# Kernel optimization log

Measured on AMD Instinct MI355X. Metric: run time of the kernel, lower is better.

## Reference

```python
import jax, jax.numpy as jnp
import numpy as np

B, N, C = 128, 2048, 3
VL, PN = 256, 128  # vector_length, prediction_num
NEG_SLOPE = 0.01   # torch LeakyReLU default
BN_EPS = 1e-5


def _lin(key, fin, fout):
    k1, k2 = jax.random.split(key)
    lim = 1.0 / np.sqrt(fin)
    W = jax.random.uniform(k1, (fin, fout), minval=-lim, maxval=lim, dtype=jnp.float32)
    b = jax.random.uniform(k2, (fout,), minval=-lim, maxval=lim, dtype=jnp.float32)
    return W, b


def setup_inputs() -> dict:
    key = jax.random.key(0)
    ks = jax.random.split(key, 14)
    x = jax.random.normal(ks[0], (B, N, C), dtype=jnp.float32)
    lengths = jnp.maximum(jax.random.randint(ks[1], (B,), 0, N), 1).astype(jnp.int32)
    eps = jax.random.normal(ks[2], (B, VL), dtype=jnp.float32)
    W1, b1 = _lin(ks[3], C, 64)
    W2, b2 = _lin(ks[4], 64, 64)
    W3, b3 = _lin(ks[5], 64, 128)
    W4, b4 = _lin(ks[6], 128, 1024)
    Wf, bf = _lin(ks[7], 1024, 1024)
    Wmu, bmu = _lin(ks[8], 1024, VL)
    Wlv, blv = _lin(ks[9], 1024, VL)
    Wd1, bd1 = _lin(ks[10], VL, 1024)
    Wd2, bd2 = _lin(ks[11], 1024, 1024)
    Wd3, bd3 = _lin(ks[12], 1024, PN * C)
    g1 = jnp.ones((1024,), jnp.float32); be1 = jnp.zeros((1024,), jnp.float32)
    g2 = jnp.ones((1024,), jnp.float32); be2 = jnp.zeros((1024,), jnp.float32)
    return dict(x=x, lengths=lengths, eps=eps,
                W1=W1, b1=b1, W2=W2, b2=b2, W3=W3, b3=b3, W4=W4, b4=b4,
                Wf=Wf, bf=bf, Wmu=Wmu, bmu=bmu, Wlv=Wlv, blv=blv,
                Wd1=Wd1, bd1=bd1, g1=g1, be1=be1,
                Wd2=Wd2, bd2=bd2, g2=g2, be2=be2,
                Wd3=Wd3, bd3=bd3)


def _lrelu(h):
    return jnp.where(h > 0, h, NEG_SLOPE * h)


def _bn(h, g, b):
    # BatchNorm1d in training mode: biased batch stats
    m = h.mean(axis=0)
    v = h.var(axis=0)
    return (h - m) * jax.lax.rsqrt(v + BN_EPS) * g + b


def reference(x, lengths, eps,
              W1, b1, W2, b2, W3, b3, W4, b4,
              Wf, bf, Wmu, bmu, Wlv, blv,
              Wd1, bd1, g1, be1, Wd2, bd2, g2, be2, Wd3, bd3):
    # --- pointnet per-point MLP (batched over padded [B,N,C]) ---
    h = _lrelu(x @ W1 + b1)          # [B,N,64]
    h = _lrelu(h @ W2 + b2)          # [B,N,64]
    h = _lrelu(h @ W3 + b3)          # [B,N,128]
    h = _lrelu(h @ W4 + b4)          # [B,N,1024]
    # masked max over points (ragged -> padded+mask)
    mask = jnp.arange(N)[None, :] < lengths[:, None]   # [B,N]
    h = jnp.where(mask[:, :, None], h, -jnp.inf)
    pooled = jnp.max(h, axis=1)      # [B,1024]
    # --- encoder head ---
    e = _lrelu(pooled @ Wf + bf)
    mu = e @ Wmu + bmu               # [B,VL]
    logvar = e @ Wlv + blv           # [B,VL]
    # --- reparameterize ---
    z = mu + eps * jnp.exp(0.5 * logvar)
    # --- decoder: Linear+BN+LeakyReLU x2, final Linear ---
    d = _lrelu(_bn(z @ Wd1 + bd1, g1, be1))
    d = _lrelu(_bn(d @ Wd2 + bd2, g2, be2))
    y = (d @ Wd3 + bd3).reshape(-1, PN, C)   # [B,PN,C]
    return (y, mu, logvar)
```

## Files before the change

### kernel.cpp

```cpp
#include <hip/hip_runtime.h>
#include <hip/hip_bf16.h>
#include <math.h>

#define NEG_SLOPE 0.01f

typedef short short8 __attribute__((ext_vector_type(8)));
typedef float f32x4 __attribute__((ext_vector_type(4)));

__device__ __forceinline__ float lrelu(float v) { return v > 0.0f ? v : NEG_SLOPE * v; }

__device__ __forceinline__ short f2bf(float f) {
    __hip_bfloat16 h = __float2bfloat16(f);
    return __builtin_bit_cast(short, h);
}

__global__ __launch_bounds__(256) void pack_all(
    const float* __restrict__ W4, const float* __restrict__ Wf,
    const float* __restrict__ Wmu, const float* __restrict__ Wlv,
    const float* __restrict__ Wd1, const float* __restrict__ Wd2,
    const float* __restrict__ Wd3, const float* __restrict__ W2,
    const float* __restrict__ W3,
    short* __restrict__ F4, short* __restrict__ Ff, short* __restrict__ Fmuvl,
    short* __restrict__ Fd1, short* __restrict__ Fd2, short* __restrict__ Fd3,
    short* __restrict__ F2, short* __restrict__ F3)
{
    int bid = blockIdx.x;
    const float* src = nullptr; short* dst = nullptr; int K = 0, N = 0; int muvl = 0;
    if      (bid < 64)   { src = W4;  dst = F4;    K = 128;  N = 1024; }
    else if (bid < 576)  { src = Wf;  dst = Ff;    K = 1024; N = 1024; bid -= 64; }
    else if (bid < 832)  { src = nullptr; dst = Fmuvl; K = 1024; N = 512; muvl = 1; bid -= 576; }
    else if (bid < 960)  { src = Wd1; dst = Fd1;   K = 256;  N = 1024; bid -= 832; }
    else if (bid < 1472) { src = Wd2; dst = Fd2;   K = 1024; N = 1024; bid -= 960; }
    else if (bid < 1664) { src = Wd3; dst = Fd3;   K = 1024; N = 384;  bid -= 1472; }
    else if (bid < 1666) { src = W2;  dst = F2;    K = 64;   N = 64;   bid -= 1664; }
    else                 { src = W3;  dst = F3;    K = 64;   N = 128;  bid -= 1666; }

    const int fragid = bid * 4 + (threadIdx.x >> 6);
    const int lane   = threadIdx.x & 63;
    const int K32    = K >> 5;
    const int t   = fragid / (K32 * 4);
    const int rem = fragid - t * K32 * 4;
    const int ks  = rem >> 2;
    const int n   = rem & 3;
    const int col   = t * 64 + n * 16 + (lane & 15);
    const int kbase = ks * 32 + (lane >> 4) * 8;

    short8 v;
#pragma unroll
    for (int e = 0; e < 8; ++e) {
        float f;
        if (muvl) f = (col < 256) ? Wmu[(size_t)(kbase + e) * 256 + col]
                                  : Wlv[(size_t)(kbase + e) * 256 + col - 256];
        else      f = src[(size_t)(kbase + e) * N + col];
        v[e] = f2bf(f);
    }
    *(short8*)&dst[(size_t)fragid * 512 + lane * 8] = v;
}

__global__ __launch_bounds__(128, 2) void h3_kernel(
    const float* __restrict__ x, const int* __restrict__ lengths,
    const float* __restrict__ W1, const float* __restrict__ b1,
    const float* __restrict__ b2, const float* __restrict__ b3,
    const short* __restrict__ F2, const short* __restrict__ F3,
    short* __restrict__ h3p)
{
    const int tid  = threadIdx.x;
    const int b    = blockIdx.x & 127;
    const int c2   = blockIdx.x >> 7;
    const int lane = tid & 63;
    const int w    = tid >> 6;
    const int g    = c2 * 2 + w;
    const int len  = lengths[b];
    if (g * 64 >= len) return;

    __shared__ short S[16384];
    short* Aw = S + w * 8192;
    const int gid = b * 2048 + g * 64 + lane;

    {
        const float x0 = x[gid * 3 + 0];
        const float x1 = x[gid * 3 + 1];
        const float x2 = x[gid * 3 + 2];
#pragma unroll
        for (int q = 0; q < 8; ++q) {
            short8 pv;
#pragma unroll
            for (int e = 0; e < 8; ++e) {
                int c = q * 8 + e;
                float v = b1[c];
                v = fmaf(x0, W1[c], v);
                v = fmaf(x1, W1[64 + c], v);
                v = fmaf(x2, W1[128 + c], v);
                pv[e] = f2bf(lrelu(v));
            }
            *(short8*)&Aw[lane * 64 + ((q ^ (lane & 7)) * 8)] = pv;
        }
    }

    {
        short8 a2[4][2];
#pragma unroll
        for (int m = 0; m < 4; ++m)
#pragma unroll
            for (int ks = 0; ks < 2; ++ks) {
                int rl = m * 16 + (lane & 15);
                int kch = ks * 4 + (lane >> 4);
                a2[m][ks] = *(const short8*)&Aw[rl * 64 + ((kch ^ (rl & 7)) * 8)];
            }
        short8 b2f[2][4];
#pragma unroll
        for (int ks = 0; ks < 2; ++ks)
#pragma unroll
            for (int n = 0; n < 4; ++n)
                b2f[ks][n] = *(const short8*)&F2[(size_t)(ks * 4 + n) * 512 + lane * 8];

        f32x4 acc2[4][4];
#pragma unroll
        for (int m = 0; m < 4; ++m)
#pragma unroll
            for (int n = 0; n < 4; ++n) acc2[m][n] = 0;
#pragma unroll
        for (int ks = 0; ks < 2; ++ks)
#pragma unroll
            for (int n = 0; n < 4; ++n)
#pragma unroll
                for (int m = 0; m < 4; ++m)
                    acc2[m][n] = __builtin_amdgcn_mfma_f32_16x16x32_bf16(
                        a2[m][ks], b2f[ks][n], acc2[m][n], 0, 0, 0);

#pragma unroll
        for (int n = 0; n < 4; ++n) {
            int col = n * 16 + (lane & 15);
            float bv = b2[col];
            int colch = col >> 3;
#pragma unroll
            for (int m = 0; m < 4; ++m)
#pragma unroll
                for (int r = 0; r < 4; ++r) {
                    int rl = m * 16 + (lane >> 4) * 4 + r;
                    Aw[4096 + rl * 64 + ((colch ^ (rl & 7)) * 8) + (col & 7)] =
                        f2bf(lrelu(acc2[m][n][r] + bv));
                }
        }
    }

    {
        short8 a3[4][2];
#pragma unroll
        for (int m = 0; m < 4; ++m)
#pragma unroll
            for (int ks = 0; ks < 2; ++ks) {
                int rl = m * 16 + (lane & 15);
                int kch = ks * 4 + (lane >> 4);
                a3[m][ks] = *(const short8*)&Aw[4096 + rl * 64 + ((kch ^ (rl & 7)) * 8)];
            }
#pragma unroll
        for (int half = 0; half < 2; ++half) {
            short8 b3f[2][4];
#pragma unroll
            for (int ks = 0; ks < 2; ++ks)
#pragma unroll
                for (int n = 0; n < 4; ++n)
                    b3f[ks][n] = *(const short8*)&F3[(size_t)(half * 8 + ks * 4 + n) * 512 + lane * 8];

            f32x4 acc3[4][4];
#pragma unroll
            for (int m = 0; m < 4; ++m)
#pragma unroll
                for (int n = 0; n < 4; ++n) acc3[m][n] = 0;
#pragma unroll
            for (int ks = 0; ks < 2; ++ks)
#pragma unroll
                for (int n = 0; n < 4; ++n)
#pragma unroll
                    for (int m = 0; m < 4; ++m)
                        acc3[m][n] = __builtin_amdgcn_mfma_f32_16x16x32_bf16(
                            a3[m][ks], b3f[ks][n], acc3[m][n], 0, 0, 0);

#pragma unroll
            for (int n = 0; n < 4; ++n) {
                int col = half * 64 + n * 16 + (lane & 15);
                float bv = b3[col];
                int colch = col >> 3;
#pragma unroll
                for (int m = 0; m < 4; ++m)
#pragma unroll
                    for (int r = 0; r < 4; ++r) {
                        int rl = m * 16 + (lane >> 4) * 4 + r;
                        Aw[rl * 128 + ((colch ^ (rl & 7)) * 8) + (col & 7)] =
                            f2bf(lrelu(acc3[m][n][r] + bv));
                    }
            }
        }
    }

    const size_t obase = ((size_t)(b * 32 + g) * 16) * 512 + lane * 8;
#pragma unroll
    for (int ks = 0; ks < 4; ++ks)
#pragma unroll
        for (int m = 0; m < 4; ++m) {
            int rl = m * 16 + (lane & 15);
            int ch = (ks * 4 + (lane >> 4)) ^ (rl & 7);
            short8 af = *(const short8*)&Aw[rl * 128 + ch * 8];
            *(short8*)&h3p[obase + (size_t)(ks * 4 + m) * 512] = af;
        }
}

__global__ __launch_bounds__(256, 3) void l4_pool_kernel(
    const short* __restrict__ h3p, const int* __restrict__ lengths,
    const short* __restrict__ F4, float* __restrict__ part)
{
    const int tid = threadIdx.x, lane = tid & 63, w = tid >> 6;
    const int b = blockIdx.x, ch = blockIdx.y, rs = blockIdx.z;
    const int len = lengths[b];
    const int live64 = (len + 63) >> 6;
    const int cbeg = rs * 4;
    int cend = cbeg + 4; if (cend > live64) cend = live64;
    if (cbeg >= cend) return;

    __shared__ short L[16384];

    const int t = ch * 4 + w;
    short8 bfr[4][4];
#pragma unroll
    for (int ks = 0; ks < 4; ++ks)
#pragma unroll
        for (int n = 0; n < 4; ++n)
            bfr[ks][n] = *(const short8*)&F4[(size_t)((t * 4 + ks) * 4 + n) * 512 + lane * 8];

    const int partial = (len & 63) ? (live64 - 1) : -1;
    const int rem = len & 63;

    f32x4 rmax[4];
#pragma unroll
    for (int n = 0; n < 4; ++n)
#pragma unroll
        for (int rr = 0; rr < 4; ++rr) rmax[n][rr] = -INFINITY;

    const size_t bb = (size_t)b * 32;
    short8 stg[4];
    {
        const size_t fb = (bb + cbeg) * 16 * 512;
#pragma unroll
        for (int pass = 0; pass < 4; ++pass)
            stg[pass] = *(const short8*)&h3p[fb + (size_t)(pass * 256 + tid) * 8];
#pragma unroll
        for (int pass = 0; pass < 4; ++pass)
            *(short8*)&L[(pass * 256 + tid) * 8] = stg[pass];
    }
    __syncthreads();

    for (int c = cbeg; c < cend; ++c) {
        const int p = (c - cbeg) & 1;
        if (c + 1 < cend) {
            const size_t fb = (bb + c + 1) * 16 * 512;
#pragma unroll
            for (int pass = 0; pass < 4; ++pass)
                stg[pass] = *(const short8*)&h3p[fb + (size_t)(pass * 256 + tid) * 8];
        }

        const short* Lb = L + p * 8192;
#pragma unroll
        for (int mh = 0; mh < 2; ++mh) {
            f32x4 acc[2][4];
#pragma unroll
            for (int j = 0; j < 2; ++j)
#pragma unroll
                for (int n = 0; n < 4; ++n) acc[j][n] = 0;
#pragma unroll
            for (int ks = 0; ks < 4; ++ks) {
                short8 a0 = *(const short8*)&Lb[(ks * 4 + mh * 2 + 0) * 512 + lane * 8];
                short8 a1 = *(const short8*)&Lb[(ks * 4 + mh * 2 + 1) * 512 + lane * 8];
#pragma unroll
                for (int n = 0; n < 4; ++n) {
                    acc[0][n] = __builtin_amdgcn_mfma_f32_16x16x32_bf16(a0, bfr[ks][n], acc[0][n], 0, 0, 0);
                    acc[1][n] = __builtin_amdgcn_mfma_f32_16x16x32_bf16(a1, bfr[ks][n], acc[1][n], 0, 0, 0);
                }
            }
            if (c == partial) {
#pragma unroll
                for (int j = 0; j < 2; ++j)
#pragma unroll
                    for (int n = 0; n < 4; ++n)
#pragma unroll
                        for (int rr = 0; rr < 4; ++rr) {
                            int row = mh * 32 + j * 16 + (lane >> 4) * 4 + rr;
                            rmax[n][rr] = fmaxf(rmax[n][rr],
                                (row < rem) ? acc[j][n][rr] : -INFINITY);
                        }
            } else {
#pragma unroll
                for (int j = 0; j < 2; ++j)
#pragma unroll
                    for (int n = 0; n < 4; ++n)
#pragma unroll
                        for (int rr = 0; rr < 4; ++rr)
                            rmax[n][rr] = fmaxf(rmax[n][rr], acc[j][n][rr]);
            }
        }

        if (c + 1 < cend) {
            short* Ln = L + (p ^ 1) * 8192;
#pragma unroll
            for (int pass = 0; pass < 4; ++pass)
                *(short8*)&Ln[(pass * 256 + tid) * 8] = stg[pass];
        }
        __syncthreads();
    }

#pragma unroll
    for (int n = 0; n < 4; ++n) {
        float v = fmaxf(fmaxf(rmax[n][0], rmax[n][1]), fmaxf(rmax[n][2], rmax[n][3]));
        v = fmaxf(v, __shfl_xor(v, 16));
        v = fmaxf(v, __shfl_xor(v, 32));
        if (lane < 16)
            part[((size_t)b * 8 + rs) * 1024 + ch * 256 + w * 64 + n * 16 + lane] = v;
    }
}

__global__ __launch_bounds__(256) void reduce_pool_kernel(
    const float* __restrict__ part, const int* __restrict__ lengths,
    const float* __restrict__ b4, short* __restrict__ pooled)
{
    const int b = blockIdx.x;
    const int nlive = (lengths[b] + 255) >> 8;
    for (int i = threadIdx.x; i < 1024; i += 256) {
        float m = part[((size_t)b * 8 + 0) * 1024 + i];
        for (int j = 1; j < nlive; ++j)
            m = fmaxf(m, part[((size_t)b * 8 + j) * 1024 + i]);
        pooled[(size_t)b * 1024 + i] = f2bf(lrelu(m + b4[i]));
    }
}

template<int K32, int EPI>
__global__ __launch_bounds__(64) void gemm16(
    const short* __restrict__ A, const short* __restrict__ Wfrag,
    const float* __restrict__ bias, const float* __restrict__ bias2,
    float* __restrict__ outF, float* __restrict__ outF2,
    short* __restrict__ outB, int Nout)
{
    const int lane = threadIdx.x;
    const int cbb = blockIdx.x, rh = blockIdx.y;
    const int K = K32 * 32;
    const int t = cbb >> 2, n = cbb & 3;

    short8 bf[K32];
#pragma unroll
    for (int ks = 0; ks < K32; ++ks)
        bf[ks] = *(const short8*)&Wfrag[(size_t)((t * K32 + ks) * 4 + n) * 512 + lane * 8];

    const int arow0 = rh * 32 + (lane & 15);
    const int koff  = (lane >> 4) * 8;
    f32x4 acc[2];
    acc[0] = 0; acc[1] = 0;
#pragma unroll
    for (int ks = 0; ks < K32; ++ks) {
        short8 a0 = *(const short8*)&A[(size_t)arow0 * K + ks * 32 + koff];
        short8 a1 = *(const short8*)&A[(size_t)(arow0 + 16) * K + ks * 32 + koff];
        acc[0] = __builtin_amdgcn_mfma_f32_16x16x32_bf16(a0, bf[ks], acc[0], 0, 0, 0);
        acc[1] = __builtin_amdgcn_mfma_f32_16x16x32_bf16(a1, bf[ks], acc[1], 0, 0, 0);
    }

    const int c0 = cbb * 16;
    const int cl = lane & 15;
    if (EPI == 2) {
        const float* bs = (c0 < 256) ? bias : bias2;
        float* of = (c0 < 256) ? outF : outF2;
        int col = (c0 & 255) + cl;
        float bv = bs[col];
#pragma unroll
        for (int m = 0; m < 2; ++m)
#pragma unroll
            for (int rr = 0; rr < 4; ++rr) {
                int row = rh * 32 + m * 16 + (lane >> 4) * 4 + rr;
                of[(size_t)row * 256 + col] = acc[m][rr] + bv;
            }
    } else {
        int col = c0 + cl;
        float bv = bias[col];
#pragma unroll
        for (int m = 0; m < 2; ++m)
#pragma unroll
            for (int rr = 0; rr < 4; ++rr) {
                int row = rh * 32 + m * 16 + (lane >> 4) * 4 + rr;
                float v = acc[m][rr] + bv;
                if (EPI == 1) outB[(size_t)row * Nout + col] = f2bf(lrelu(v));
                else          outF[(size_t)row * Nout + col] = v;
            }
    }
}

template<int K32, bool ZIN>
__global__ __launch_bounds__(256) void gemmBN(
    const short* __restrict__ A, const float* __restrict__ muv,
    const float* __restrict__ lvv, const float* __restrict__ eps,
    const short* __restrict__ Wfrag,
    const float* __restrict__ g, const float* __restrict__ be,
    short* __restrict__ outB, int Nout)
{
    __shared__ float bns[4][16];
    __shared__ float bnq[4][16];

    const int tid = threadIdx.x, lane = tid & 63, w = tid >> 6;
    const int cbb = blockIdx.x;
    const int K = K32 * 32;
    const int t = cbb >> 2, n = cbb & 3;

    short8 bf[K32];
#pragma unroll
    for (int ks = 0; ks < K32; ++ks)
        bf[ks] = *(const short8*)&Wfrag[(size_t)((t * K32 + ks) * 4 + n) * 512 + lane * 8];

    const int arow0 = w * 32 + (lane & 15);
    const int koff  = (lane >> 4) * 8;
    f32x4 acc[2];
    acc[0] = 0; acc[1] = 0;
#pragma unroll
    for (int ks = 0; ks < K32; ++ks) {
        short8 a0, a1;
        if (ZIN) {
#pragma unroll
            for (int e = 0; e < 8; ++e) {
                int k = ks * 32 + koff + e;
                size_t i0 = (size_t)arow0 * 256 + k;
                size_t i1 = (size_t)(arow0 + 16) * 256 + k;
                a0[e] = f2bf(fmaf(eps[i0], expf(0.5f * lvv[i0]), muv[i0]));
                a1[e] = f2bf(fmaf(eps[i1], expf(0.5f * lvv[i1]), muv[i1]));
            }
        } else {
            a0 = *(const short8*)&A[(size_t)arow0 * K + ks * 32 + koff];
            a1 = *(const short8*)&A[(size_t)(arow0 + 16) * K + ks * 32 + koff];
        }
        acc[0] = __builtin_amdgcn_mfma_f32_16x16x32_bf16(a0, bf[ks], acc[0], 0, 0, 0);
        acc[1] = __builtin_amdgcn_mfma_f32_16x16x32_bf16(a1, bf[ks], acc[1], 0, 0, 0);
    }

    float s = 0.f, q = 0.f;
#pragma unroll
    for (int m = 0; m < 2; ++m)
#pragma unroll
        for (int rr = 0; rr < 4; ++rr) {
            float v = acc[m][rr];
            s += v; q = fmaf(v, v, q);
        }
    s += __shfl_xor(s, 16); s += __shfl_xor(s, 32);
    q += __shfl_xor(q, 16); q += __shfl_xor(q, 32);
    if (lane < 16) { bns[w][lane] = s; bnq[w][lane] = q; }
    __syncthreads();

    const int cl = lane & 15;
    float st = bns[0][cl] + bns[1][cl] + bns[2][cl] + bns[3][cl];
    float qt = bnq[0][cl] + bnq[1][cl] + bnq[2][cl] + bnq[3][cl];
    float mean = st * (1.0f / 128.0f);
    float var  = qt * (1.0f / 128.0f) - mean * mean;
    float rs   = 1.0f / sqrtf(var + 1e-5f);
    const int col = cbb * 16 + cl;
    float gg = g[col] * rs;
    float bb = be[col] - mean * gg;

#pragma unroll
    for (int m = 0; m < 2; ++m)
#pragma unroll
        for (int rr = 0; rr < 4; ++rr) {
            int row = w * 32 + m * 16 + (lane >> 4) * 4 + rr;
            outB[(size_t)row * Nout + col] = f2bf(lrelu(fmaf(acc[m][rr], gg, bb)));
        }
}

extern "C" void kernel_launch(void* const* d_in, const int* in_sizes, int n_in,
                              void* d_out, int out_size, void* d_ws, size_t ws_size,
                              hipStream_t stream)
{
    const float* x       = (const float*)d_in[0];
    const int*   lengths = (const int*)  d_in[1];
    const float* eps     = (const float*)d_in[2];
    const float* W1  = (const float*)d_in[3];  const float* b1  = (const float*)d_in[4];
    const float* W2  = (const float*)d_in[5];  const float* b2  = (const float*)d_in[6];
    const float* W3  = (const float*)d_in[7];  const float* b3  = (const float*)d_in[8];
    const float* W4  = (const float*)d_in[9];  const float* b4  = (const float*)d_in[10];
    const float* Wf  = (const float*)d_in[11]; const float* bf  = (const float*)d_in[12];
    const float* Wmu = (const float*)d_in[13]; const float* bmu = (const float*)d_in[14];
    const float* Wlv = (const float*)d_in[15]; const float* blv = (const float*)d_in[16];
    const float* Wd1 = (const float*)d_in[17];
    const float* g1  = (const float*)d_in[19]; const float* be1 = (const float*)d_in[20];
    const float* Wd2 = (const float*)d_in[21];
    const float* g2  = (const float*)d_in[23]; const float* be2 = (const float*)d_in[24];
    const float* Wd3 = (const float*)d_in[25]; const float* bd3 = (const float*)d_in[26];

    float* out = (float*)d_out;
    float* y_out  = out;
    float* mu_out = out + 49152;
    float* lv_out = out + 81920;

    char* ws = (char*)d_ws;
    short* F4    = (short*)(ws + 0);
    short* Ff    = (short*)(ws + 262144);
    short* Fmuvl = (short*)(ws + 2359296);
    short* Fd1   = (short*)(ws + 3407872);
    short* Fd2   = (short*)(ws + 3932160);
    short* Fd3   = (short*)(ws + 6029312);
    short* F2    = (short*)(ws + 6815744);
    short* F3    = (short*)(ws + 6823936);
    short* h3p   = (short*)(ws + 6840320);
    float* part  = (float*)(ws + 73949184);
    short* pooled = (short*)(ws + 6840320 + 0);
    short* ebuf   = (short*)(ws + 6840320 + 262144);
    short* d1v    = (short*)(ws + 6840320 + 524288);
    short* d2v    = (short*)(ws + 6840320 + 786432);

    pack_all<<<1670, 256, 0, stream>>>(W4, Wf, Wmu, Wlv, Wd1, Wd2, Wd3, W2, W3,
                                       F4, Ff, Fmuvl, Fd1, Fd2, Fd3, F2, F3);
    h3_kernel<<<2048, 128, 0, stream>>>(x, lengths, W1, b1, b2, b3, F2, F3, h3p);
    l4_pool_kernel<<<dim3(128, 4, 8), 256, 0, stream>>>(h3p, lengths, F4, part);
    reduce_pool_kernel<<<128, 256, 0, stream>>>(part, lengths, b4, pooled);
    gemm16<32, 1><<<dim3(64, 4), 64, 0, stream>>>(pooled, Ff, bf, nullptr,
                                                  nullptr, nullptr, ebuf, 1024);
    gemm16<32, 2><<<dim3(32, 4), 64, 0, stream>>>(ebuf, Fmuvl, bmu, blv,
                                                  mu_out, lv_out, nullptr, 256);
    gemmBN<8, true><<<64, 256, 0, stream>>>(nullptr, mu_out, lv_out, eps,
                                            Fd1, g1, be1, d1v, 1024);
    gemmBN<32, false><<<64, 256, 0, stream>>>(d1v, nullptr, nullptr, nullptr,
                                              Fd2, g2, be2, d2v, 1024);
    gemm16<32, 0><<<dim3(24, 4), 64, 0, stream>>>(d2v, Fd3, bd3, nullptr,
                                                  y_out, nullptr, nullptr, 384);
}
```

Measured before the change: 120.2 us.

## Load point chunk once into LDS and loop over all output channel groups per block

The l4_pool kernel no longer splits the 1024 output channels across a grid dimension. Each block now stages all (up to 4) 64-point chunks of h3 into a 64KB LDS buffer once, then loops over the four channel groups, reloading the W4 fragments for each. This removes the fourfold re-reading of h3 from global memory and the per-chunk double-buffer sync. In exchange the grid shrinks fourfold, LDS use doubles, occupancy drops to 2 blocks per CU, and load/compute overlap is lost.

```diff
diff --git a/kernel.cpp b/kernel.cpp
--- a/kernel.cpp
+++ b/kernel.cpp
@@ -206,115 +206,102 @@
         }
 }
 
-__global__ __launch_bounds__(256, 3) void l4_pool_kernel(
+__global__ __launch_bounds__(256, 2) void l4_pool_kernel(
     const short* __restrict__ h3p, const int* __restrict__ lengths,
     const short* __restrict__ F4, float* __restrict__ part)
 {
     const int tid = threadIdx.x, lane = tid & 63, w = tid >> 6;
-    const int b = blockIdx.x, ch = blockIdx.y, rs = blockIdx.z;
+    const int b  = blockIdx.x & 127;
+    const int rs = blockIdx.x >> 7;
     const int len = lengths[b];
     const int live64 = (len + 63) >> 6;
     const int cbeg = rs * 4;
     int cend = cbeg + 4; if (cend > live64) cend = live64;
     if (cbeg >= cend) return;
-
-    __shared__ short L[16384];
-
-    const int t = ch * 4 + w;
-    short8 bfr[4][4];
-#pragma unroll
-    for (int ks = 0; ks < 4; ++ks)
-#pragma unroll
-        for (int n = 0; n < 4; ++n)
-            bfr[ks][n] = *(const short8*)&F4[(size_t)((t * 4 + ks) * 4 + n) * 512 + lane * 8];
+    const int nch = cend - cbeg;
+
+    __shared__ short L[32768];
+
+    const size_t bb = (size_t)b * 32;
+    for (int ci = 0; ci < nch; ++ci) {
+        const size_t fb = (bb + cbeg + ci) * 16 * 512;
+#pragma unroll
+        for (int pass = 0; pass < 4; ++pass) {
+            short8 v = *(const short8*)&h3p[fb + (size_t)(pass * 256 + tid) * 8];
+            *(short8*)&L[ci * 8192 + (pass * 256 + tid) * 8] = v;
+        }
+    }
+    __syncthreads();
 
     const int partial = (len & 63) ? (live64 - 1) : -1;
     const int rem = len & 63;
 
-    f32x4 rmax[4];
-#pragma unroll
-    for (int n = 0; n < 4; ++n)
-#pragma unroll
-        for (int rr = 0; rr < 4; ++rr) rmax[n][rr] = -INFINITY;
-
-    const size_t bb = (size_t)b * 32;
-    short8 stg[4];
-    {
-        const size_t fb = (bb + cbeg) * 16 * 512;
-#pragma unroll
-        for (int pass = 0; pass < 4; ++pass)
-            stg[pass] = *(const short8*)&h3p[fb + (size_t)(pass * 256 + tid) * 8];
-#pragma unroll
-        for (int pass = 0; pass < 4; ++pass)
-            *(short8*)&L[(pass * 256 + tid) * 8] = stg[pass];
-    }
-    __syncthreads();
-
-    for (int c = cbeg; c < cend; ++c) {
-        const int p = (c - cbeg) & 1;
-        if (c + 1 < cend) {
-            const size_t fb = (bb + c + 1) * 16 * 512;
-#pragma unroll
-            for (int pass = 0; pass < 4; ++pass)
-                stg[pass] = *(const short8*)&h3p[fb + (size_t)(pass * 256 + tid) * 8];
-        }
-
-        const short* Lb = L + p * 8192;
-#pragma unroll
-        for (int mh = 0; mh < 2; ++mh) {
-            f32x4 acc[2][4];
-#pragma unroll
-            for (int j = 0; j < 2; ++j)
-#pragma unroll
-                for (int n = 0; n < 4; ++n) acc[j][n] = 0;
-#pragma unroll
-            for (int ks = 0; ks < 4; ++ks) {
-                short8 a0 = *(const short8*)&Lb[(ks * 4 + mh * 2 + 0) * 512 + lane * 8];
-                short8 a1 = *(const short8*)&Lb[(ks * 4 + mh * 2 + 1) * 512 + lane * 8];
-#pragma unroll
-                for (int n = 0; n < 4; ++n) {
-                    acc[0][n] = __builtin_amdgcn_mfma_f32_16x16x32_bf16(a0, bfr[ks][n], acc[0][n], 0, 0, 0);
-                    acc[1][n] = __builtin_amdgcn_mfma_f32_16x16x32_bf16(a1, bfr[ks][n], acc[1][n], 0, 0, 0);
+    for (int ch = 0; ch < 4; ++ch) {
+        const int t = ch * 4 + w;
+        short8 bfr[4][4];
+#pragma unroll
+        for (int ks = 0; ks < 4; ++ks)
+#pragma unroll
+            for (int n = 0; n < 4; ++n)
+                bfr[ks][n] = *(const short8*)&F4[(size_t)((t * 4 + ks) * 4 + n) * 512 + lane * 8];
+
+        f32x4 rmax[4];
+#pragma unroll
+        for (int n = 0; n < 4; ++n)
+#pragma unroll
+            for (int rr = 0; rr < 4; ++rr) rmax[n][rr] = -INFINITY;
+
+        for (int ci = 0; ci < nch; ++ci) {
+            const short* Lb = L + ci * 8192;
+            const bool isPartial = (cbeg + ci) == partial;
+#pragma unroll
+            for (int mh = 0; mh < 2; ++mh) {
+                f32x4 acc[2][4];
+#pragma unroll
+                for (int j = 0; j < 2; ++j)
+#pragma unroll
+                    for (int n = 0; n < 4; ++n) acc[j][n] = 0;
+#pragma unroll
+                for (int ks = 0; ks < 4; ++ks) {
+                    short8 a0 = *(const short8*)&Lb[(ks * 4 + mh * 2 + 0) * 512 + lane * 8];
+                    short8 a1 = *(const short8*)&Lb[(ks * 4 + mh * 2 + 1) * 512 + lane * 8];
+#pragma unroll
+                    for (int n = 0; n < 4; ++n) {
+                        acc[0][n] = __builtin_amdgcn_mfma_f32_16x16x32_bf16(a0, bfr[ks][n], acc[0][n], 0, 0, 0);
+                        acc[1][n] = __builtin_amdgcn_mfma_f32_16x16x32_bf16(a1, bfr[ks][n], acc[1][n], 0, 0, 0);
+                    }
                 }
-            }
-            if (c == partial) {
-#pragma unroll
-                for (int j = 0; j < 2; ++j)
-#pragma unroll
-                    for (int n = 0; n < 4; ++n)
-#pragma unroll
-                        for (int rr = 0; rr < 4; ++rr) {
-                            int row = mh * 32 + j * 16 + (lane >> 4) * 4 + rr;
-                            rmax[n][rr] = fmaxf(rmax[n][rr],
-                                (row < rem) ? acc[j][n][rr] : -INFINITY);
-                        }
-            } else {
-#pragma unroll
-                for (int j = 0; j < 2; ++j)
-#pragma unroll
-                    for (int n = 0; n < 4; ++n)
-#pragma unroll
-                        for (int rr = 0; rr < 4; ++rr)
-                            rmax[n][rr] = fmaxf(rmax[n][rr], acc[j][n][rr]);
-            }
-        }
-
-        if (c + 1 < cend) {
-            short* Ln = L + (p ^ 1) * 8192;
-#pragma unroll
-            for (int pass = 0; pass < 4; ++pass)
-                *(short8*)&Ln[(pass * 256 + tid) * 8] = stg[pass];
-        }
-        __syncthreads();
-    }
-
-#pragma unroll
-    for (int n = 0; n < 4; ++n) {
-        float v = fmaxf(fmaxf(rmax[n][0], rmax[n][1]), fmaxf(rmax[n][2], rmax[n][3]));
-        v = fmaxf(v, __shfl_xor(v, 16));
-        v = fmaxf(v, __shfl_xor(v, 32));
-        if (lane < 16)
-            part[((size_t)b * 8 + rs) * 1024 + ch * 256 + w * 64 + n * 16 + lane] = v;
+                if (isPartial) {
+#pragma unroll
+                    for (int j = 0; j < 2; ++j)
+#pragma unroll
+                        for (int n = 0; n < 4; ++n)
+#pragma unroll
+                            for (int rr = 0; rr < 4; ++rr) {
+                                int row = mh * 32 + j * 16 + (lane >> 4) * 4 + rr;
+                                rmax[n][rr] = fmaxf(rmax[n][rr],
+                                    (row < rem) ? acc[j][n][rr] : -INFINITY);
+                            }
+                } else {
+#pragma unroll
+                    for (int j = 0; j < 2; ++j)
+#pragma unroll
+                        for (int n = 0; n < 4; ++n)
+#pragma unroll
+                            for (int rr = 0; rr < 4; ++rr)
+                                rmax[n][rr] = fmaxf(rmax[n][rr], acc[j][n][rr]);
+                }
+            }
+        }
+
+#pragma unroll
+        for (int n = 0; n < 4; ++n) {
+            float v = fmaxf(fmaxf(rmax[n][0], rmax[n][1]), fmaxf(rmax[n][2], rmax[n][3]));
+            v = fmaxf(v, __shfl_xor(v, 16));
+            v = fmaxf(v, __shfl_xor(v, 32));
+            if (lane < 16)
+                part[((size_t)b * 8 + rs) * 1024 + ch * 256 + w * 64 + n * 16 + lane] = v;
+        }
     }
 }
 
@@ -511,7 +498,7 @@
     pack_all<<<1670, 256, 0, stream>>>(W4, Wf, Wmu, Wlv, Wd1, Wd2, Wd3, W2, W3,
                                        F4, Ff, Fmuvl, Fd1, Fd2, Fd3, F2, F3);
     h3_kernel<<<2048, 128, 0, stream>>>(x, lengths, W1, b1, b2, b3, F2, F3, h3p);
-    l4_pool_kernel<<<dim3(128, 4, 8), 256, 0, stream>>>(h3p, lengths, F4, part);
+    l4_pool_kernel<<<1024, 256, 0, stream>>>(h3p, lengths, F4, part);
     reduce_pool_kernel<<<128, 256, 0, stream>>>(part, lengths, b4, pooled);
     gemm16<32, 1><<<dim3(64, 4), 64, 0, stream>>>(pooled, Ff, bf, nullptr,
                                                   nullptr, nullptr, ebuf, 1024);
```

Measured after the change: 126.1 us. 5.0% more time.
